# Performance work log

Hardware: AMD Instinct MI355X
Metric: run time of the kernel (lower is better)

Reference implementation:

```python
import jax, jax.numpy as jnp
import numpy as np

NC = 151  # number of object classes (VG)
NR = 51   # number of relation classes (VG)


def setup_inputs() -> dict:
    key = jax.random.key(0)
    ks = jax.random.split(key, 10)
    B, N, D = 32, 100, 4096
    H = D // 4
    w = lambda k, shape, fan_in: (jax.random.normal(k, shape, jnp.float32) / np.sqrt(fan_in).astype(np.float32))
    return {
        "encoder_reps": jax.random.normal(ks[0], (B * N, D), jnp.float32),
        "W_comp": w(ks[1], (D, H), D),        # obj_comp Linear (no bias)
        "W_ou1": w(ks[2], (H, H), H),         # ou1 Linear
        "W_ofc": w(ks[3], (H, H), H),         # ofc_u Linear
        "W_decomp": w(ks[4], (H, D), H),      # obj_decomp Linear
        "conv1": w(ks[5], (10, NR, 3, 3), NR * 9),  # Conv2d(51,10,3,pad=1)
        "conv2": w(ks[6], (5, 10, 3, 3), 10 * 9),   # Conv2d(10,5,3,pad=1)
        "conv3": w(ks[7], (1, 5, 1, 1), 5),         # Conv2d(5,1,1)
        "freq_emb": jax.random.normal(ks[8], (NC * NC, NR), jnp.float32) * 0.01,
        "obj_preds": jax.random.randint(ks[9], (B * N,), 0, NC),
        "num_obj": 100,
    }


def reference(encoder_reps, W_comp, W_ou1, W_ofc, W_decomp, conv1, conv2, conv3, freq_emb, obj_preds, num_obj):
    T, D = encoder_reps.shape
    N = num_obj
    B = T // N
    relu = jax.nn.relu
    # obj_comp then per-image ou1 (vectorized over images)
    comp = relu(encoder_reps @ W_comp).reshape(B, N, -1)   # [B,N,H]
    obj_u1 = relu(comp @ W_ou1)                             # [B,N,H]
    # product-index frequency-bias gather: emb[subj*NC + obj]
    labels = obj_preds.reshape(B, N)
    pair_idx = labels[:, :, None] * NC + labels[:, None, :]  # [B,N,N]
    adj_fg = freq_emb[pair_idx]                               # [B,N,N,NR]
    # adjacency net: Conv-Conv-Conv-Tanh over the NxN 'image' with NR channels
    x = jnp.transpose(adj_fg, (0, 3, 1, 2))                   # [B,NR,N,N]
    dn = ("NCHW", "OIHW", "NCHW")
    x = jax.lax.conv_general_dilated(x, conv1, (1, 1), "SAME", dimension_numbers=dn)
    x = jax.lax.conv_general_dilated(x, conv2, (1, 1), "SAME", dimension_numbers=dn)
    x = jnp.tanh(jax.lax.conv_general_dilated(x, conv3, (1, 1), "SAME", dimension_numbers=dn))
    adj = x[:, 0]                                             # [B,N,N]
    # graph message passing: adj @ obj_u1, then ofc_u / decomp + residual
    ofl_u = jnp.einsum("bnm,bmh->bnh", adj, obj_u1).reshape(T, -1)
    u_m = relu(ofl_u @ W_ofc)
    decomp = relu(u_m @ W_decomp)
    return decomp + encoder_reps
```

## Files before the change

### kernel.cpp

```cpp
#include <hip/hip_runtime.h>
#include <cmath>

#define NCC 151
#define NRCH 51
#define BDIM 32
#define NOBJ 100
#define DDIM 4096
#define HDIM 1024
#define TDIM (BDIM * NOBJ)

typedef __bf16 bf16_t;
typedef __bf16 bf16x8 __attribute__((ext_vector_type(8)));
typedef __bf16 bf16x4 __attribute__((ext_vector_type(4)));
typedef float f32x4 __attribute__((ext_vector_type(4)));

template <bool RELU, bool ADDBF16, int SPLITK, int MODE>
__global__ __launch_bounds__(256) void gemm_bf16(
    const bf16_t* __restrict__ A,
    const bf16_t* __restrict__ Bt,
    const bf16_t* __restrict__ add,
    void* __restrict__ Cout,
    int N, int K, size_t MN) {
  __shared__ __align__(16) bf16_t Asm[128 * 64];
  __shared__ __align__(16) bf16_t Bsm[128 * 64];
  const int tid = threadIdx.x;
  const int lane = tid & 63;
  const int w = tid >> 6;
  const int wm = w >> 1, wn = w & 1;

  const int nx = gridDim.x, ny = gridDim.y, nz = gridDim.z;
  const int h = blockIdx.x + nx * (blockIdx.y + ny * blockIdx.z);
  int bx, by, bz;
  if (MODE == 1) {
    bz = h & 7;
    const int s = h >> 3;
    by = s % ny;
    bx = s / ny;
  } else if (MODE == 3) {
    const int xcd = h & 7, s = h >> 3;
    bz = xcd >> 1;
    const int half = xcd & 1;
    if (half == 1 && s >= 96) return;
    const int c = s / 40;
    if (c < 2) {
      const int within = s % 40;
      bx = within / 5;
      by = (half ? 13 : 0) + c * 5 + within % 5;
    } else if (half == 0) {
      const int w2 = s - 80;
      bx = w2 / 3;
      by = 10 + w2 % 3;
    } else {
      const int w2 = s - 80;
      bx = w2 / 2;
      by = 23 + w2 % 2;
    }
  } else {
    const int nwg = nx * ny * nz;
    const int q = nwg >> 3;
    const int lin = (h & 7) * q + (h >> 3);
    by = lin % ny;
    const int r = lin / ny;
    bx = r % nx;
    bz = r / nx;
  }

  const int bm = by * 128, bn = bx * 128;
  const int lr = lane & 15;
  const int lk = lane >> 4;

  int kBeg = 0, kEnd = K;
  if (SPLITK > 1) {
    const int chunk = (((K / 64) + SPLITK - 1) / SPLITK) * 64;
    kBeg = bz * chunk;
    kEnd = min(K, kBeg + chunk);
  }

  f32x4 acc[4][4];
#pragma unroll
  for (int m = 0; m < 4; ++m)
#pragma unroll
    for (int n = 0; n < 4; ++n) acc[m][n] = (f32x4){0.f, 0.f, 0.f, 0.f};

  const int srow = tid >> 3;
  const int sslot = tid & 7;

  char* ldsA = (char*)Asm;
  char* ldsB = (char*)Bsm;

  for (int kt = kBeg; kt < kEnd; kt += 64) {
    __syncthreads();
#pragma unroll
    for (int i = 0; i < 4; ++i) {
      const int row = i * 32 + srow;
      const int kc = sslot ^ (row & 7);
      const bf16_t* ga = A + (size_t)(bm + row) * K + kt + kc * 8;
      const bf16_t* gb = Bt + (size_t)(bn + row) * K + kt + kc * 8;
      __builtin_amdgcn_global_load_lds(
          (const __attribute__((address_space(1))) void*)ga,
          (__attribute__((address_space(3))) void*)(ldsA + i * 4096 + w * 1024),
          16, 0, 0);
      __builtin_amdgcn_global_load_lds(
          (const __attribute__((address_space(1))) void*)gb,
          (__attribute__((address_space(3))) void*)(ldsB + i * 4096 + w * 1024),
          16, 0, 0);
    }
    __syncthreads();

    bf16x8 af[4][2], bfr[4][2];
#pragma unroll
    for (int m = 0; m < 4; ++m) {
      const int row = wm * 64 + m * 16 + lr;
#pragma unroll
      for (int kk = 0; kk < 2; ++kk) {
        const int slot = kk * 4 + lk;
        af[m][kk] =
            *(const bf16x8*)(ldsA + row * 128 + ((slot ^ (lr & 7)) << 4));
      }
    }
#pragma unroll
    for (int n = 0; n < 4; ++n) {
      const int row = wn * 64 + n * 16 + lr;
#pragma unroll
      for (int kk = 0; kk < 2; ++kk) {
        const int slot = kk * 4 + lk;
        bfr[n][kk] =
            *(const bf16x8*)(ldsB + row * 128 + ((slot ^ (lr & 7)) << 4));
      }
    }
#pragma unroll
    for (int m = 0; m < 4; ++m)
#pragma unroll
      for (int n = 0; n < 4; ++n) {
        acc[m][n] = __builtin_amdgcn_mfma_f32_16x16x32_bf16(
            af[m][0], bfr[n][0], acc[m][n], 0, 0, 0);
        acc[m][n] = __builtin_amdgcn_mfma_f32_16x16x32_bf16(
            af[m][1], bfr[n][1], acc[m][n], 0, 0, 0);
      }
  }

  const int or0 = bm + wm * 64 + lk * 4;
  const int oc0 = bn + wn * 64 + lr;
#pragma unroll
  for (int m = 0; m < 4; ++m)
#pragma unroll
    for (int n = 0; n < 4; ++n)
#pragma unroll
      for (int r = 0; r < 4; ++r) {
        float v = acc[m][n][r];
        const size_t off = (size_t)(or0 + m * 16 + r) * N + (oc0 + n * 16);
        if (SPLITK > 1) {
          ((bf16_t*)Cout)[bz * MN + off] = (bf16_t)v;
        } else {
          if (RELU) v = fmaxf(v, 0.f);
          if (ADDBF16)
            ((float*)Cout)[off] = v + (float)add[off];
          else
            ((bf16_t*)Cout)[off] = (bf16_t)v;
        }
      }
}

template <int NPART>
__global__ __launch_bounds__(256) void reduceN_kernel(
    const bf16_t* __restrict__ p, bf16_t* __restrict__ out, int n8,
    size_t MN) {
  int i = blockIdx.x * 256 + threadIdx.x;
  if (i >= n8) return;
  float s[8] = {};
#pragma unroll
  for (int z = 0; z < NPART; ++z) {
    bf16x8 v = *(const bf16x8*)(p + z * MN + (size_t)i * 8);
#pragma unroll
    for (int j = 0; j < 8; ++j) s[j] += (float)v[j];
  }
  bf16x8 o;
#pragma unroll
  for (int j = 0; j < 8; ++j) o[j] = (bf16_t)fmaxf(s[j], 0.f);
  *(bf16x8*)(out + (size_t)i * 8) = o;
}

__global__ __launch_bounds__(256) void cvt_bf16_kernel(
    const float* __restrict__ in, bf16_t* __restrict__ out, int n4) {
  int i = blockIdx.x * 256 + threadIdx.x;
  if (i >= n4) return;
  float4 v = ((const float4*)in)[i];
  bf16x4 o = {(bf16_t)v.x, (bf16_t)v.y, (bf16_t)v.z, (bf16_t)v.w};
  ((bf16x4*)out)[i] = o;
}

__global__ __launch_bounds__(256) void transT_kernel(
    const float* __restrict__ in, bf16_t* __restrict__ out, int K, int N) {
  __shared__ float t[32][33];
  const int n0 = blockIdx.x * 32, k0 = blockIdx.y * 32;
  const int tx = threadIdx.x & 31, ty = threadIdx.x >> 5;
#pragma unroll
  for (int i = 0; i < 4; ++i)
    t[ty + i * 8][tx] = in[(size_t)(k0 + ty + i * 8) * N + n0 + tx];
  __syncthreads();
#pragma unroll
  for (int i = 0; i < 4; ++i)
    out[(size_t)(n0 + ty + i * 8) * K + k0 + tx] = (bf16_t)t[tx][ty + i * 8];
}

__global__ __launch_bounds__(256) void prep_w1r_kernel(
    const float* __restrict__ w1, float* __restrict__ w1r) {
  int idx = blockIdx.x * 256 + threadIdx.x;
  if (idx >= NRCH * 90) return;
  int ci = idx / 90, r = idx % 90, k9 = r / 10, co = r % 10;
  w1r[idx] = w1[((co * NRCH + ci) * 3 + k9 / 3) * 3 + (k9 % 3)];
}

__global__ __launch_bounds__(128) void prep_w23_kernel(
    const float* __restrict__ w2, const float* __restrict__ w3,
    float* __restrict__ w23) {
  int t = threadIdx.x;
  if (t >= 90) return;
  int k9 = t / 10, c2 = t % 10;
  float acc = 0.f;
#pragma unroll
  for (int c3 = 0; c3 < 5; ++c3)
    acc += w3[c3] * w2[((c3 * 10 + c2) * 3 + k9 / 3) * 3 + (k9 % 3)];
  w23[t] = acc;
}

__global__ __launch_bounds__(256) void pidx_kernel(
    const int* __restrict__ preds, int* __restrict__ pidx) {
  int idx = blockIdx.x * 256 + threadIdx.x;
  if (idx >= BDIM * NOBJ * NOBJ) return;
  int j = idx % NOBJ;
  int i = (idx / NOBJ) % NOBJ;
  int b = idx / (NOBJ * NOBJ);
  pidx[idx] = preds[b * NOBJ + i] * NCC + preds[b * NOBJ + j];
}

__global__ __launch_bounds__(128) void femb1_kernel(
    const float* __restrict__ femb, const float* __restrict__ w1r,
    float* __restrict__ femb1) {
  __shared__ float row[NRCH];
  const int p = blockIdx.x;
  if (threadIdx.x < NRCH)
    row[threadIdx.x] = femb[(size_t)p * NRCH + threadIdx.x];
  __syncthreads();
  const int t = threadIdx.x;
  if (t >= 90) return;
  float acc = 0.f;
#pragma unroll
  for (int ci = 0; ci < NRCH; ++ci) acc += row[ci] * w1r[ci * 90 + t];
  femb1[((size_t)p * 9 + t / 10) * 12 + (t % 10)] = acc;
}

__global__ __launch_bounds__(256) void conv1g_kernel(
    const int* __restrict__ pidx, const float* __restrict__ femb1,
    float* __restrict__ x1) {
  int idx = blockIdx.x * 256 + threadIdx.x;
  if (idx >= BDIM * NOBJ * NOBJ) return;
  int j = idx % NOBJ;
  int i = (idx / NOBJ) % NOBJ;
  int b = idx / (NOBJ * NOBJ);
  f32x4 a0 = {0.f, 0.f, 0.f, 0.f}, a1 = a0, a2 = a0;
  const int* pb = pidx + b * NOBJ * NOBJ;
#pragma unroll
  for (int kh = 0; kh < 3; ++kh) {
    int ii = i + kh - 1;
    if (ii < 0 || ii >= NOBJ) continue;
#pragma unroll
    for (int kw = 0; kw < 3; ++kw) {
      int jj = j + kw - 1;
      if (jj < 0 || jj >= NOBJ) continue;
      int p = pb[ii * NOBJ + jj];
      const f32x4* f =
          (const f32x4*)(femb1 + ((size_t)p * 9 + kh * 3 + kw) * 12);
      a0 += f[0];
      a1 += f[1];
      a2 += f[2];
    }
  }
  f32x4* o = (f32x4*)(x1 + (size_t)idx * 12);
  o[0] = a0;
  o[1] = a1;
  o[2] = a2;
}

__global__ __launch_bounds__(256) void conv23_kernel(
    const float* __restrict__ x1, const float* __restrict__ w23,
    float* __restrict__ adj) {
  __shared__ float w[90];
  if (threadIdx.x < 90) w[threadIdx.x] = w23[threadIdx.x];
  __syncthreads();
  int idx = blockIdx.x * 256 + threadIdx.x;
  if (idx >= BDIM * NOBJ * NOBJ) return;
  int j = idx % NOBJ;
  int i = (idx / NOBJ) % NOBJ;
  int b = idx / (NOBJ * NOBJ);
  float acc = 0.f;
  const float* xb = x1 + (size_t)b * NOBJ * NOBJ * 12;
#pragma unroll
  for (int kh = 0; kh < 3; ++kh) {
    int ii = i + kh - 1;
    if (ii < 0 || ii >= NOBJ) continue;
#pragma unroll
    for (int kw = 0; kw < 3; ++kw) {
      int jj = j + kw - 1;
      if (jj < 0 || jj >= NOBJ) continue;
      const float* xr = xb + (ii * NOBJ + jj) * 12;
      const float* wr = w + (kh * 3 + kw) * 10;
#pragma unroll
      for (int c = 0; c < 10; ++c) acc += wr[c] * xr[c];
    }
  }
  adj[idx] = tanhf(acc);
}

__global__ __launch_bounds__(256) void einsum_mfma_kernel(
    const float* __restrict__ adj,
    const bf16_t* __restrict__ u1,
    bf16_t* __restrict__ ofl) {
  __shared__ __align__(16) bf16_t As[128 * 128];
  __shared__ __align__(16) bf16_t Us[128 * 128];
  const int b = blockIdx.y;
  const int h0 = blockIdx.x * 128;
  const int tid = threadIdx.x, lane = tid & 63, w = tid >> 6;
  const int wm = w >> 1, wn = w & 1;
  const int lr = lane & 15, lk = lane >> 4;

  {
    f32x4 z = {0.f, 0.f, 0.f, 0.f};
#pragma unroll
    for (int i = 0; i < 8; ++i) ((f32x4*)As)[tid + i * 256] = z;
#pragma unroll
    for (int i = 0; i < 8; ++i) ((f32x4*)Us)[tid + i * 256] = z;
  }
  __syncthreads();

  const float* ab = adj + (size_t)b * 10000;
#pragma unroll
  for (int i = 0; i < 10; ++i) {
    int idx = tid + i * 256;
    if (idx < 2500) {
      int row = idx / 25, kc = idx % 25;
      f32x4 v = ((const f32x4*)ab)[idx];
      bf16x4 o = {(bf16_t)v[0], (bf16_t)v[1], (bf16_t)v[2], (bf16_t)v[3]};
      int slot = kc >> 1;
      *(bf16x4*)((char*)As + row * 256 + ((slot ^ (row & 7)) << 4) +
                 (kc & 1) * 8) = o;
    }
  }

  const bf16_t* ub = u1 + (size_t)b * 100 * HDIM + h0;
#pragma unroll
  for (int i = 0; i < 7; ++i) {
    int idx = tid + i * 256;
    if (idx < 1600) {
      int hc = idx / 100, m = idx % 100;
      bf16x8 v = *(const bf16x8*)(ub + (size_t)m * HDIM + hc * 8);
      int slot = m >> 3, mr = m & 7;
#pragma unroll
      for (int j = 0; j < 8; ++j) {
        int h = hc * 8 + j;
        *((bf16_t*)((char*)Us + h * 256 + ((slot ^ (h & 7)) << 4) + mr * 2)) =
            v[j];
      }
    }
  }
  __syncthreads();

  f32x4 acc[4][4];
#pragma unroll
  for (int m = 0; m < 4; ++m)
#pragma unroll
    for (int n = 0; n < 4; ++n) acc[m][n] = (f32x4){0.f, 0.f, 0.f, 0.f};

#pragma unroll
  for (int ks = 0; ks < 4; ++ks) {
    bf16x8 a[4], u[4];
#pragma unroll
    for (int m = 0; m < 4; ++m) {
      int row = wm * 64 + m * 16 + lr;
      int slot = ks * 4 + lk;
      a[m] = *(const bf16x8*)((char*)As + row * 256 + ((slot ^ (lr & 7)) << 4));
    }
#pragma unroll
    for (int n = 0; n < 4; ++n) {
      int row = wn * 64 + n * 16 + lr;
      int slot = ks * 4 + lk;
      u[n] = *(const bf16x8*)((char*)Us + row * 256 + ((slot ^ (lr & 7)) << 4));
    }
#pragma unroll
    for (int m = 0; m < 4; ++m)
#pragma unroll
      for (int n = 0; n < 4; ++n)
        acc[m][n] = __builtin_amdgcn_mfma_f32_16x16x32_bf16(a[m], u[n],
                                                            acc[m][n], 0, 0, 0);
  }

  const int or0 = wm * 64 + lk * 4;
  const int oc0 = h0 + wn * 64 + lr;
#pragma unroll
  for (int m = 0; m < 4; ++m)
#pragma unroll
    for (int n = 0; n < 4; ++n)
#pragma unroll
      for (int r = 0; r < 4; ++r) {
        int row = or0 + m * 16 + r;
        if (row < 100)
          ofl[((size_t)b * 100 + row) * HDIM + oc0 + n * 16] =
              (bf16_t)acc[m][n][r];
      }
}

extern "C" void kernel_launch(void* const* d_in, const int* in_sizes, int n_in,
                              void* d_out, int out_size, void* d_ws,
                              size_t ws_size, hipStream_t stream) {
  const float* enc = (const float*)d_in[0];
  const float* W_comp = (const float*)d_in[1];
  const float* W_ou1 = (const float*)d_in[2];
  const float* W_ofc = (const float*)d_in[3];
  const float* W_dec = (const float*)d_in[4];
  const float* conv1w = (const float*)d_in[5];
  const float* conv2w = (const float*)d_in[6];
  const float* conv3w = (const float*)d_in[7];
  const float* femb = (const float*)d_in[8];
  const int* preds = (const int*)d_in[9];
  float* out = (float*)d_out;
  char* wsb = (char*)d_ws;

  const size_t MN = (size_t)TDIM * HDIM;

  bf16_t* encb   = (bf16_t*)(wsb + 0);
  bf16_t* WcompT = (bf16_t*)(wsb + 26214400);
  bf16_t* comp   = (bf16_t*)(wsb + 34603008);
  bf16_t* part4  = (bf16_t*)(wsb + 41156608);
  bf16_t* Wou1T  = (bf16_t*)(wsb + 41156608);
  float*  w1r    = (float*)(wsb + 43253760);
  float*  w23    = (float*)(wsb + 43272128);
  float*  femb1  = (float*)(wsb + 43272512);
  int*    pidx   = (int*)(wsb + 53122560);
  float*  x1     = (float*)(wsb + 54402560);
  bf16_t* obj_u1 = (bf16_t*)(wsb + 69762560);
  float*  adj    = (float*)(wsb + 76316160);
  bf16_t* ofl_u  = (bf16_t*)(wsb + 26214400);
  bf16_t* WofcT  = (bf16_t*)(wsb + 32768000);
  bf16_t* u_m    = (bf16_t*)(wsb + 34865152);
  bf16_t* WdecT  = (bf16_t*)(wsb + 41418752);

  const int n8 = (int)(MN / 8);

  cvt_bf16_kernel<<<(TDIM * DDIM / 4 + 255) / 256, 256, 0, stream>>>(
      enc, encb, TDIM * DDIM / 4);
  transT_kernel<<<dim3(HDIM / 32, DDIM / 32), 256, 0, stream>>>(
      W_comp, WcompT, DDIM, HDIM);

  gemm_bf16<false, false, 4, 3><<<dim3(832, 1, 1), 256, 0, stream>>>(
      encb, WcompT, nullptr, part4, HDIM, DDIM, MN);
  reduceN_kernel<4><<<n8 / 256, 256, 0, stream>>>(part4, comp, n8, MN);

  transT_kernel<<<dim3(HDIM / 32, HDIM / 32), 256, 0, stream>>>(
      W_ou1, Wou1T, HDIM, HDIM);
  gemm_bf16<true, false, 1, 0>
      <<<dim3(HDIM / 128, TDIM / 128), 256, 0, stream>>>(
          comp, Wou1T, nullptr, obj_u1, HDIM, HDIM, MN);

  prep_w1r_kernel<<<(NRCH * 90 + 255) / 256, 256, 0, stream>>>(conv1w, w1r);
  prep_w23_kernel<<<1, 128, 0, stream>>>(conv2w, conv3w, w23);
  pidx_kernel<<<(BDIM * NOBJ * NOBJ + 255) / 256, 256, 0, stream>>>(preds,
                                                                    pidx);
  femb1_kernel<<<NCC * NCC, 128, 0, stream>>>(femb, w1r, femb1);

  conv1g_kernel<<<(BDIM * NOBJ * NOBJ + 255) / 256, 256, 0, stream>>>(
      pidx, femb1, x1);
  conv23_kernel<<<(BDIM * NOBJ * NOBJ + 255) / 256, 256, 0, stream>>>(x1, w23,
                                                                      adj);

  transT_kernel<<<dim3(HDIM / 32, HDIM / 32), 256, 0, stream>>>(
      W_ofc, WofcT, HDIM, HDIM);
  transT_kernel<<<dim3(DDIM / 32, HDIM / 32), 256, 0, stream>>>(
      W_dec, WdecT, HDIM, DDIM);

  einsum_mfma_kernel<<<dim3(HDIM / 128, BDIM), 256, 0, stream>>>(adj, obj_u1,
                                                                 ofl_u);

  gemm_bf16<true, false, 1, 0>
      <<<dim3(HDIM / 128, TDIM / 128), 256, 0, stream>>>(
          ofl_u, WofcT, nullptr, u_m, HDIM, HDIM, MN);

  gemm_bf16<true, true, 1, 0>
      <<<dim3(DDIM / 128, TDIM / 128), 256, 0, stream>>>(
          u_m, WdecT, encb, out, DDIM, HDIM, MN);
}
```

Before: 249.2 us.

## Double-buffer GEMM LDS tiles and fold small prep kernels into consumers

The bf16 GEMM now keeps two LDS buffers and issues the next k-tile's global-to-LDS loads before running MFMAs on the current tile, dropping one barrier per iteration. Separately, the weight-permutation, conv2/conv3 fusion and pair-index kernels are removed: femb1 reads conv1 weights directly, conv23 builds its fused weights in shared memory, and conv1g computes pair indices from the label vector. This cuts several tiny launches and a 1.28MB index buffer, at the cost of doubling GEMM LDS (64KB per block), which may lower occupancy. The unused MODE 1 swizzle path is also dropped.

New measurement: 353.6 us. 41.9% more time.

```diff
diff --git a/kernel.cpp b/kernel.cpp
--- a/kernel.cpp
+++ b/kernel.cpp
@@ -21,8 +21,8 @@
     const bf16_t* __restrict__ add,
     void* __restrict__ Cout,
     int N, int K, size_t MN) {
-  __shared__ __align__(16) bf16_t Asm[128 * 64];
-  __shared__ __align__(16) bf16_t Bsm[128 * 64];
+  __shared__ __align__(16) bf16_t Asm[2][128 * 64];
+  __shared__ __align__(16) bf16_t Bsm[2][128 * 64];
   const int tid = threadIdx.x;
   const int lane = tid & 63;
   const int w = tid >> 6;
@@ -31,12 +31,7 @@
   const int nx = gridDim.x, ny = gridDim.y, nz = gridDim.z;
   const int h = blockIdx.x + nx * (blockIdx.y + ny * blockIdx.z);
   int bx, by, bz;
-  if (MODE == 1) {
-    bz = h & 7;
-    const int s = h >> 3;
-    by = s % ny;
-    bx = s / ny;
-  } else if (MODE == 3) {
+  if (MODE == 3) {
     const int xcd = h & 7, s = h >> 3;
     bz = xcd >> 1;
     const int half = xcd & 1;
@@ -85,11 +80,7 @@
   const int srow = tid >> 3;
   const int sslot = tid & 7;
 
-  char* ldsA = (char*)Asm;
-  char* ldsB = (char*)Bsm;
-
-  for (int kt = kBeg; kt < kEnd; kt += 64) {
-    __syncthreads();
+  auto stage = [&](int buf, int kt) {
 #pragma unroll
     for (int i = 0; i < 4; ++i) {
       const int row = i * 32 + srow;
@@ -98,15 +89,27 @@
       const bf16_t* gb = Bt + (size_t)(bn + row) * K + kt + kc * 8;
       __builtin_amdgcn_global_load_lds(
           (const __attribute__((address_space(1))) void*)ga,
-          (__attribute__((address_space(3))) void*)(ldsA + i * 4096 + w * 1024),
+          (__attribute__((address_space(3))) void*)((char*)&Asm[buf][0] +
+                                                    i * 4096 + w * 1024),
           16, 0, 0);
       __builtin_amdgcn_global_load_lds(
           (const __attribute__((address_space(1))) void*)gb,
-          (__attribute__((address_space(3))) void*)(ldsB + i * 4096 + w * 1024),
+          (__attribute__((address_space(3))) void*)((char*)&Bsm[buf][0] +
+                                                    i * 4096 + w * 1024),
           16, 0, 0);
     }
-    __syncthreads();
-
+  };
+
+  stage(0, kBeg);
+  __syncthreads();
+
+  int cur = 0;
+  for (int kt = kBeg; kt < kEnd; kt += 64) {
+    const bool more = (kt + 64 < kEnd);
+    if (more) stage(cur ^ 1, kt + 64);
+
+    char* ldsA = (char*)&Asm[cur][0];
+    char* ldsB = (char*)&Bsm[cur][0];
     bf16x8 af[4][2], bfr[4][2];
 #pragma unroll
     for (int m = 0; m < 4; ++m) {
@@ -137,6 +140,9 @@
         acc[m][n] = __builtin_amdgcn_mfma_f32_16x16x32_bf16(
             af[m][1], bfr[n][1], acc[m][n], 0, 0, 0);
       }
+
+    if (more) __syncthreads();
+    cur ^= 1;
   }
 
   const int or0 = bm + wm * 64 + lk * 4;
@@ -203,39 +209,9 @@
     out[(size_t)(n0 + ty + i * 8) * K + k0 + tx] = (bf16_t)t[tx][ty + i * 8];
 }
 
-__global__ __launch_bounds__(256) void prep_w1r_kernel(
-    const float* __restrict__ w1, float* __restrict__ w1r) {
-  int idx = blockIdx.x * 256 + threadIdx.x;
-  if (idx >= NRCH * 90) return;
-  int ci = idx / 90, r = idx % 90, k9 = r / 10, co = r % 10;
-  w1r[idx] = w1[((co * NRCH + ci) * 3 + k9 / 3) * 3 + (k9 % 3)];
-}
-
-__global__ __launch_bounds__(128) void prep_w23_kernel(
-    const float* __restrict__ w2, const float* __restrict__ w3,
-    float* __restrict__ w23) {
-  int t = threadIdx.x;
-  if (t >= 90) return;
-  int k9 = t / 10, c2 = t % 10;
-  float acc = 0.f;
-#pragma unroll
-  for (int c3 = 0; c3 < 5; ++c3)
-    acc += w3[c3] * w2[((c3 * 10 + c2) * 3 + k9 / 3) * 3 + (k9 % 3)];
-  w23[t] = acc;
-}
-
-__global__ __launch_bounds__(256) void pidx_kernel(
-    const int* __restrict__ preds, int* __restrict__ pidx) {
-  int idx = blockIdx.x * 256 + threadIdx.x;
-  if (idx >= BDIM * NOBJ * NOBJ) return;
-  int j = idx % NOBJ;
-  int i = (idx / NOBJ) % NOBJ;
-  int b = idx / (NOBJ * NOBJ);
-  pidx[idx] = preds[b * NOBJ + i] * NCC + preds[b * NOBJ + j];
-}
 
 __global__ __launch_bounds__(128) void femb1_kernel(
-    const float* __restrict__ femb, const float* __restrict__ w1r,
+    const float* __restrict__ femb, const float* __restrict__ w1,
     float* __restrict__ femb1) {
   __shared__ float row[NRCH];
   const int p = blockIdx.x;
@@ -244,22 +220,30 @@
   __syncthreads();
   const int t = threadIdx.x;
   if (t >= 90) return;
+  const int k9 = t / 10, co = t % 10;
   float acc = 0.f;
 #pragma unroll
-  for (int ci = 0; ci < NRCH; ++ci) acc += row[ci] * w1r[ci * 90 + t];
-  femb1[((size_t)p * 9 + t / 10) * 12 + (t % 10)] = acc;
+  for (int ci = 0; ci < NRCH; ++ci)
+    acc += row[ci] * w1[(co * NRCH + ci) * 9 + k9];
+  femb1[((size_t)p * 9 + k9) * 12 + co] = acc;
 }
 
 __global__ __launch_bounds__(256) void conv1g_kernel(
-    const int* __restrict__ pidx, const float* __restrict__ femb1,
+    const int* __restrict__ preds, const float* __restrict__ femb1,
     float* __restrict__ x1) {
   int idx = blockIdx.x * 256 + threadIdx.x;
   if (idx >= BDIM * NOBJ * NOBJ) return;
   int j = idx % NOBJ;
   int i = (idx / NOBJ) % NOBJ;
   int b = idx / (NOBJ * NOBJ);
+  const int* pr = preds + b * NOBJ;
+  int li[3], lj[3];
+#pragma unroll
+  for (int d = 0; d < 3; ++d) {
+    li[d] = pr[min(max(i + d - 1, 0), NOBJ - 1)];
+    lj[d] = pr[min(max(j + d - 1, 0), NOBJ - 1)];
+  }
   f32x4 a0 = {0.f, 0.f, 0.f, 0.f}, a1 = a0, a2 = a0;
-  const int* pb = pidx + b * NOBJ * NOBJ;
 #pragma unroll
   for (int kh = 0; kh < 3; ++kh) {
     int ii = i + kh - 1;
@@ -268,7 +252,7 @@
     for (int kw = 0; kw < 3; ++kw) {
       int jj = j + kw - 1;
       if (jj < 0 || jj >= NOBJ) continue;
-      int p = pb[ii * NOBJ + jj];
+      int p = li[kh] * NCC + lj[kw];
       const f32x4* f =
           (const f32x4*)(femb1 + ((size_t)p * 9 + kh * 3 + kw) * 12);
       a0 += f[0];
@@ -283,10 +267,17 @@
 }
 
 __global__ __launch_bounds__(256) void conv23_kernel(
-    const float* __restrict__ x1, const float* __restrict__ w23,
-    float* __restrict__ adj) {
+    const float* __restrict__ x1, const float* __restrict__ w2,
+    const float* __restrict__ w3, float* __restrict__ adj) {
   __shared__ float w[90];
-  if (threadIdx.x < 90) w[threadIdx.x] = w23[threadIdx.x];
+  if (threadIdx.x < 90) {
+    const int k9 = threadIdx.x / 10, c2 = threadIdx.x % 10;
+    float a = 0.f;
+#pragma unroll
+    for (int c3 = 0; c3 < 5; ++c3)
+      a += w3[c3] * w2[(c3 * 10 + c2) * 9 + k9];
+    w[threadIdx.x] = a;
+  }
   __syncthreads();
   int idx = blockIdx.x * 256 + threadIdx.x;
   if (idx >= BDIM * NOBJ * NOBJ) return;
@@ -432,10 +423,7 @@
   bf16_t* comp   = (bf16_t*)(wsb + 34603008);
   bf16_t* part4  = (bf16_t*)(wsb + 41156608);
   bf16_t* Wou1T  = (bf16_t*)(wsb + 41156608);
-  float*  w1r    = (float*)(wsb + 43253760);
-  float*  w23    = (float*)(wsb + 43272128);
   float*  femb1  = (float*)(wsb + 43272512);
-  int*    pidx   = (int*)(wsb + 53122560);
   float*  x1     = (float*)(wsb + 54402560);
   bf16_t* obj_u1 = (bf16_t*)(wsb + 69762560);
   float*  adj    = (float*)(wsb + 76316160);
@@ -461,16 +449,11 @@
       <<<dim3(HDIM / 128, TDIM / 128), 256, 0, stream>>>(
           comp, Wou1T, nullptr, obj_u1, HDIM, HDIM, MN);
 
-  prep_w1r_kernel<<<(NRCH * 90 + 255) / 256, 256, 0, stream>>>(conv1w, w1r);
-  prep_w23_kernel<<<1, 128, 0, stream>>>(conv2w, conv3w, w23);
-  pidx_kernel<<<(BDIM * NOBJ * NOBJ + 255) / 256, 256, 0, stream>>>(preds,
-                                                                    pidx);
-  femb1_kernel<<<NCC * NCC, 128, 0, stream>>>(femb, w1r, femb1);
-
+  femb1_kernel<<<NCC * NCC, 128, 0, stream>>>(femb, conv1w, femb1);
   conv1g_kernel<<<(BDIM * NOBJ * NOBJ + 255) / 256, 256, 0, stream>>>(
-      pidx, femb1, x1);
-  conv23_kernel<<<(BDIM * NOBJ * NOBJ + 255) / 256, 256, 0, stream>>>(x1, w23,
-                                                                      adj);
+      preds, femb1, x1);
+  conv23_kernel<<<(BDIM * NOBJ * NOBJ + 255) / 256, 256, 0, stream>>>(
+      x1, conv2w, conv3w, adj);
 
   transT_kernel<<<dim3(HDIM / 32, HDIM / 32), 256, 0, stream>>>(
       W_ofc, WofcT, HDIM, HDIM);
```
